# Kernel tuning notes

Measured on AMD Instinct MI355X. Metric: run time of the kernel, lower is better.

The kernel has to match this reference:

```python
import jax, jax.numpy as jnp
import numpy as np

ROPE_BASE = 1000000.0
EPS = 1e-6
N_HEADS = 8


def apply_rope(x, base=ROPE_BASE):
    # x: [b, s, h, d]
    b, s, h, d = x.shape
    half = d // 2
    theta = 1.0 / base ** (2 * jnp.arange(half) / d)          # [half]
    angles = jnp.arange(s)[:, None] * theta[None, :]          # [s, half]
    cos = jnp.cos(angles)[None, :, None, :]                   # [1, s, 1, half]
    sin = jnp.sin(angles)[None, :, None, :]
    x1, x2 = jnp.split(x, 2, axis=-1)
    return jnp.concatenate([x1 * cos - x2 * sin, x1 * sin + x2 * cos], axis=-1)


def setup_inputs() -> dict:
    key = jax.random.key(0)
    ks = jax.random.split(key, 5)
    b, s, dim = 2, 4096, 512
    x = jax.random.normal(ks[0], (b, s, dim), dtype=jnp.float32)
    scale = jnp.ones((dim,), dtype=jnp.float32)
    init = 1.0 / np.sqrt(dim)
    Wq = jax.random.normal(ks[1], (dim, dim), dtype=jnp.float32) * init
    Wk = jax.random.normal(ks[2], (dim, dim), dtype=jnp.float32) * init
    Wv = jax.random.normal(ks[3], (dim, dim), dtype=jnp.float32) * init
    Wo = jax.random.normal(ks[4], (dim, dim), dtype=jnp.float32) * init
    return {"x": x, "scale": scale, "Wq": Wq, "Wk": Wk, "Wv": Wv, "Wo": Wo}


def reference(x, scale, Wq, Wk, Wv, Wo):
    b, s, dim = x.shape
    h = N_HEADS
    dh = dim // h
    # RMSNorm (use_fast_variance=False path)
    variance = jnp.mean(x ** 2, axis=-1, keepdims=True)
    x_norm = x / jnp.sqrt(variance + EPS) * scale
    # Projections (flax Linear: y = x @ kernel, kernel [in, out])
    q = (x_norm @ Wq).reshape(b, s, h, dh)
    k = (x_norm @ Wk).reshape(b, s, h, dh)
    v = (x_norm @ Wv).reshape(b, s, h, dh)
    q = apply_rope(q)
    k = apply_rope(k)
    scores = jnp.einsum('bthd,bshd->bhts', q, k) / jnp.sqrt(jnp.float32(dh))
    mask = jnp.triu(jnp.full((s, s), -jnp.inf, dtype=jnp.float32), k=1)
    scores = scores + mask[None, None, :, :]
    attn = jax.nn.softmax(scores, axis=-1)
    out = jnp.einsum('bhts,bshd->bthd', attn, v).reshape(b, s, dim)
    return out @ Wo
```

## Files before the change

kernel.cpp:

```cpp
#include <hip/hip_runtime.h>
#include <hip/hip_bf16.h>

typedef _Float16 f16;
typedef _Float16 f16x2 __attribute__((ext_vector_type(2)));
typedef _Float16 f16x4 __attribute__((ext_vector_type(4)));
typedef _Float16 f16x8 __attribute__((ext_vector_type(8)));
typedef float f32x4 __attribute__((ext_vector_type(4)));

#define S_LEN 4096
#define DIM   512
#define NH    8
#define DH    64
#define BATCH 2
#define BHDIM (BATCH*NH)

#define QSCALE 0.18033688011112042f

__device__ __forceinline__ void gld16(const f16* g, f16* l) {
#if __has_builtin(__builtin_amdgcn_global_load_lds)
  __builtin_amdgcn_global_load_lds((const __attribute__((address_space(1))) void*)g,
                                   (__attribute__((address_space(3))) void*)l, 16, 0, 0);
#else
  *(f16x8*)l = *(const f16x8*)g;
#endif
}

__device__ __forceinline__ float fexp2(float x) {
#if __has_builtin(__builtin_amdgcn_exp2f)
  return __builtin_amdgcn_exp2f(x);
#else
  return exp2f(x);
#endif
}

__device__ __forceinline__ f16x2 pk2(float a, float b) {
#if __has_builtin(__builtin_amdgcn_cvt_pkrtz)
  auto r = __builtin_amdgcn_cvt_pkrtz(a, b);
  f16x2 o; __builtin_memcpy(&o, &r, sizeof(o));
  return o;
#else
  f16x2 r; r[0] = (f16)a; r[1] = (f16)b; return r;
#endif
}

__global__ __launch_bounds__(256) void prep_kernel(
    const float* __restrict__ x, const float* __restrict__ scale,
    const float* __restrict__ Wq, const float* __restrict__ Wk,
    const float* __restrict__ Wv, const float* __restrict__ Wo,
    f16* __restrict__ xn, f16* __restrict__ wt_qkv, f16* __restrict__ wo_t,
    float* __restrict__ ctab, float* __restrict__ stab) {
  int bid = blockIdx.x;
  int tid = threadIdx.x;
  if (bid < 8192) {
    const float* xr = x + (size_t)bid * DIM;
    float2 v = *(const float2*)(xr + tid*2);
    float ss = v.x*v.x + v.y*v.y;
    #pragma unroll
    for (int off = 32; off > 0; off >>= 1) ss += __shfl_down(ss, off);
    __shared__ float red[4];
    if ((tid & 63) == 0) red[tid >> 6] = ss;
    __syncthreads();
    float tot = red[0] + red[1] + red[2] + red[3];
    float inv = rsqrtf(tot * (1.0f/DIM) + 1e-6f);
    float2 s = *(const float2*)(scale + tid*2);
    xn[(size_t)bid*DIM + tid*2+0] = (f16)(v.x*inv*s.x);
    xn[(size_t)bid*DIM + tid*2+1] = (f16)(v.y*inv*s.y);
  } else if (bid < 9216) {
    __shared__ f16 tile[32][33];
    int b2 = bid - 8192;
    int mat = b2 >> 8;
    int rem = b2 & 255;
    int k0 = (rem >> 4) * 32, n0 = (rem & 15) * 32;
    const float* src = (mat == 0) ? Wq : (mat == 1) ? Wk : (mat == 2) ? Wv : Wo;
    f16* dst = (mat < 3) ? (wt_qkv + (size_t)mat*DIM*DIM) : wo_t;
    int tx = tid & 31, ty = tid >> 5;
    #pragma unroll
    for (int i = 0; i < 32; i += 8)
      tile[ty+i][tx] = (f16)src[(size_t)(k0+ty+i)*DIM + n0+tx];
    __syncthreads();
    #pragma unroll
    for (int i = 0; i < 32; i += 8)
      dst[(size_t)(n0+ty+i)*DIM + k0+tx] = tile[tx][ty+i];
  } else {
    int idx = (bid - 9216)*256 + tid;
    int t = idx >> 5, d = idx & 31;
    float theta = exp2f(-(float)d * (19.931568569324174f / 32.0f));
    float sv, cv;
    sincosf((float)t * theta, &sv, &cv);
    ctab[idx] = cv; stab[idx] = sv;
  }
}

__device__ __forceinline__ void gemm128_acc(
    const f16* __restrict__ A, const f16* __restrict__ Bt,
    int m0, int n0, f16* As, f16* Bs, f32x4 (&acc)[4][4]) {
  const int tid = threadIdx.x;
  const int wave = tid >> 6, lane = tid & 63;
  const int l16 = lane & 15, quad = lane >> 4;
  const int mrow = (wave & 1) * 64, ncol = (wave >> 1) * 64;
  const int srow = tid >> 3;
  const int gc = (tid & 7) ^ ((tid >> 3) & 7);

  for (int k0 = 0; k0 < DIM; k0 += 64) {
    if (k0) __syncthreads();
    #pragma unroll
    for (int i = 0; i < 4; i++) {
      gld16(A  + (size_t)(m0 + i*32 + srow)*DIM + k0 + gc*8, As + i*2048 + tid*8);
      gld16(Bt + (size_t)(n0 + i*32 + srow)*DIM + k0 + gc*8, Bs + i*2048 + tid*8);
    }
    __syncthreads();
    #pragma unroll
    for (int kc = 0; kc < 2; kc++) {
      f16x8 a[4], b[4];
      #pragma unroll
      for (int mt = 0; mt < 4; mt++) {
        int row = mrow + mt*16 + l16;
        a[mt] = *(const f16x8*)(As + row*64 + (((quad + 4*kc) ^ (l16 & 7)) * 8));
      }
      #pragma unroll
      for (int nt = 0; nt < 4; nt++) {
        int row = ncol + nt*16 + l16;
        b[nt] = *(const f16x8*)(Bs + row*64 + (((quad + 4*kc) ^ (l16 & 7)) * 8));
      }
      #pragma unroll
      for (int mt = 0; mt < 4; mt++)
        #pragma unroll
        for (int nt = 0; nt < 4; nt++)
          acc[mt][nt] = __builtin_amdgcn_mfma_f32_16x16x32_f16(a[mt], b[nt], acc[mt][nt], 0, 0, 0);
    }
  }
}

__global__ __launch_bounds__(256) void qkv_gemm_kernel(
    const f16* __restrict__ xn, const f16* __restrict__ wt,
    const float* __restrict__ ctab, const float* __restrict__ stab,
    f16* __restrict__ qbuf, f16* __restrict__ kbuf, f16* __restrict__ vt) {
  __shared__ __align__(16) f16 As[128*64], Bs[128*64];
  int m0 = blockIdx.x * 128, n0 = blockIdx.y * 128;
  f32x4 acc[4][4] = {};
  gemm128_acc(xn, wt, m0, n0, As, Bs, acc);

  const int tid = threadIdx.x;
  const int wave = tid >> 6, lane = tid & 63;
  const int l16 = lane & 15, quad = lane >> 4;
  int ncol = n0 + (wave >> 1) * 64;
  int which = ncol >> 9;
  int head = (ncol >> 6) & 7;
  int mbase = m0 + (wave & 1) * 64;

  if (which <= 1) {
    #pragma unroll
    for (int mt = 0; mt < 4; mt++)
      #pragma unroll
      for (int nt = 0; nt < 2; nt++) {
        int d = nt*16 + l16;
        #pragma unroll
        for (int r = 0; r < 4; r++) {
          int t = (mbase + mt*16 + quad*4 + r) & 4095;
          float cv = ctab[t*32 + d], sv = stab[t*32 + d];
          float x1 = acc[mt][nt][r], x2 = acc[mt][nt+2][r];
          acc[mt][nt][r]   = x1*cv - x2*sv;
          acc[mt][nt+2][r] = x1*sv + x2*cv;
        }
      }
  }
  if (which < 2) {
    float osc = (which == 0) ? QSCALE : 1.0f;
    f16* dst = which ? kbuf : qbuf;
    #pragma unroll
    for (int mt = 0; mt < 4; mt++)
      #pragma unroll
      for (int nt = 0; nt < 4; nt++)
        #pragma unroll
        for (int r = 0; r < 4; r++) {
          int m = mbase + mt*16 + quad*4 + r;
          int b = m >> 12, t = m & 4095;
          dst[(((size_t)(b*NH + head))*S_LEN + t)*DH + nt*16 + l16] = (f16)(acc[mt][nt][r]*osc);
        }
  } else {
    #pragma unroll
    for (int mt = 0; mt < 4; mt++)
      #pragma unroll
      for (int nt = 0; nt < 4; nt++) {
        int m = mbase + mt*16 + quad*4;
        int b = m >> 12, tcol = m & 4095;
        int grp = tcol & ~63;
        int pos = ((mt >> 1)*4 + quad)*8 + (mt & 1)*4;
        int d = nt*16 + l16;
        f16x4 v4 = {(f16)acc[mt][nt][0], (f16)acc[mt][nt][1],
                    (f16)acc[mt][nt][2], (f16)acc[mt][nt][3]};
        *(f16x4*)(vt + ((size_t)((b*NH + head)*DH + d))*S_LEN + grp + pos) = v4;
      }
  }
}

__global__ __launch_bounds__(256, 4) void attn_kernel(
    const f16* __restrict__ qbuf, const f16* __restrict__ kbuf,
    const f16* __restrict__ vtb, f16* __restrict__ ao) {
  int bid = blockIdx.x;
  int bh  = bid & 15;
  int p   = bid >> 4;

  int tid = threadIdx.x;
  int wave = tid >> 6, lane = tid & 63;
  int l16 = lane & 15, quad = lane >> 4;
  int bi = wave >> 1, half = wave & 1;

  const f16* Q = qbuf + (size_t)bh*S_LEN*DH;
  const f16* K = kbuf + (size_t)bh*S_LEN*DH;
  const f16* V = vtb  + (size_t)bh*DH*S_LEN;

  int bv = bi ? p : (127 - p);
  int tc = (bv >> 1) + 1;
  int nth = ((127 - p) >> 1) + 1;
  int rbase = bv*32 + half*16;

  f16x8 qa0, qa1;
  {
    const f16* qrow = Q + (size_t)(rbase + l16)*DH + quad*8;
    qa0 = *(const f16x8*)(qrow);
    qa1 = *(const f16x8*)(qrow + 32);
  }

  f32x4 o[4] = {};
  float m_i = -1e30f;
  float l_i = 0.f;

  __shared__ __align__(16) f16 kt[2*4096];
  __shared__ __align__(16) f16 vs[2*4096];

  const int srow = tid >> 3;
  const int gcs = (tid & 7) ^ (srow & 7);

  #define STAGE(buf, kv)                                                        \
    do {                                                                        \
      f16* ktb = kt + (buf)*4096;                                               \
      f16* vsb = vs + (buf)*4096;                                               \
      _Pragma("unroll")                                                         \
      for (int n = 0; n < 2; n++) {                                             \
        gld16(K + (size_t)((kv) + n*32 + srow)*DH + gcs*8, ktb + n*2048 + tid*8);\
        gld16(V + (size_t)(n*32 + srow)*S_LEN + (kv) + gcs*8, vsb + n*2048 + tid*8);\
      }                                                                         \
    } while (0)

  STAGE(0, 0);
  __syncthreads();

  for (int it = 0; it < nth; ++it) {
    int kv0 = it * 64;
    int cur = it & 1;
    if (it + 1 < nth) STAGE(cur ^ 1, kv0 + 64);

    const f16* ktc = kt + cur*4096;
    const f16* vsc = vs + cur*4096;

    if (it < tc) {
      bool diag = (it == tc - 1);
      int ntl = diag ? ((bv & 1) ? 4 : 2) : 4;
      int kcl = ntl >> 1;

      f32x4 st[4];
      #pragma unroll
      for (int nt = 0; nt < 4; nt++) {
        if (nt >= ntl) continue;
        int row = nt*16 + l16;
        f16x8 kf0 = *(const f16x8*)(ktc + row*64 + (((quad)     ^ (row & 7))*8));
        f16x8 kf1 = *(const f16x8*)(ktc + row*64 + (((quad + 4) ^ (row & 7))*8));
        f32x4 z = {};
        z = __builtin_amdgcn_mfma_f32_16x16x32_f16(kf0, qa0, z, 0, 0, 0);
        st[nt] = __builtin_amdgcn_mfma_f32_16x16x32_f16(kf1, qa1, z, 0, 0, 0);
      }

      int qglob = rbase + l16;
      float rmx = -1e30f;
      #pragma unroll
      for (int nt = 0; nt < 4; nt++) {
        if (nt >= ntl) continue;
        if (diag) {
          int kb = kv0 + nt*16 + quad*4;
          #pragma unroll
          for (int r = 0; r < 4; r++) {
            float v = st[nt][r];
            if (kb + r > qglob) v = -1e30f;
            st[nt][r] = v;
            rmx = fmaxf(rmx, v);
          }
        } else {
          #pragma unroll
          for (int r = 0; r < 4; r++) rmx = fmaxf(rmx, st[nt][r]);
        }
      }
      rmx = fmaxf(rmx, __shfl_xor(rmx, 16));
      rmx = fmaxf(rmx, __shfl_xor(rmx, 32));
      if (!__all(rmx <= m_i + 8.0f)) {
        float mnew = fmaxf(m_i, rmx);
        float alpha = fexp2(m_i - mnew);
        m_i = mnew;
        float al[4];
        #pragma unroll
        for (int r = 0; r < 4; r++) al[r] = __shfl(alpha, quad*4 + r);
        #pragma unroll
        for (int dnt = 0; dnt < 4; dnt++)
          #pragma unroll
          for (int r = 0; r < 4; r++) o[dnt][r] *= al[r];
        l_i *= alpha;
      }
      float mref = m_i;
      float rs = 0.f;
      f16x8 pa[2];
      #pragma unroll
      for (int c = 0; c < 2; c++) {
        if (c >= kcl) continue;
        float e0 = fexp2(st[2*c  ][0] - mref);
        float e1 = fexp2(st[2*c  ][1] - mref);
        float e2 = fexp2(st[2*c  ][2] - mref);
        float e3 = fexp2(st[2*c  ][3] - mref);
        float e4 = fexp2(st[2*c+1][0] - mref);
        float e5 = fexp2(st[2*c+1][1] - mref);
        float e6 = fexp2(st[2*c+1][2] - mref);
        float e7 = fexp2(st[2*c+1][3] - mref);
        rs += ((e0+e1)+(e2+e3)) + ((e4+e5)+(e6+e7));
        f16x4 h0 = __builtin_shufflevector(pk2(e0,e1), pk2(e2,e3), 0,1,2,3);
        f16x4 h1 = __builtin_shufflevector(pk2(e4,e5), pk2(e6,e7), 0,1,2,3);
        pa[c] = __builtin_shufflevector(h0, h1, 0,1,2,3,4,5,6,7);
      }
      l_i += rs;

      #pragma unroll
      for (int c = 0; c < 2; c++) {
        if (c >= kcl) continue;
        #pragma unroll
        for (int dnt = 0; dnt < 4; dnt++) {
          int vr = dnt*16 + l16;
          f16x8 vf = *(const f16x8*)(vsc + vr*64 + (((c*4 + quad) ^ (vr & 7))*8));
          o[dnt] = __builtin_amdgcn_mfma_f32_16x16x32_f16(pa[c], vf, o[dnt], 0, 0, 0);
        }
      }
    }

    __syncthreads();
  }
  #undef STAGE

  int b = bh >> 3, h = bh & 7;
  {
    float lf = l_i;
    lf += __shfl_xor(lf, 16);
    lf += __shfl_xor(lf, 32);
    float lr[4];
    #pragma unroll
    for (int r = 0; r < 4; r++) lr[r] = __shfl(lf, quad*4 + r);
    #pragma unroll
    for (int r = 0; r < 4; r++) {
      float invl = 1.0f / lr[r];
      int t = rbase + quad*4 + r;
      size_t rowoff = ((size_t)(b*S_LEN + t))*DIM + h*DH;
      #pragma unroll
      for (int dnt = 0; dnt < 4; dnt++)
        ao[rowoff + dnt*16 + l16] = (f16)(o[dnt][r]*invl);
    }
  }
}

__global__ __launch_bounds__(256) void out_gemm_kernel(
    const f16* __restrict__ ao, const f16* __restrict__ wot,
    float* __restrict__ out) {
  __shared__ __align__(16) f16 As[128*64], Bs[128*64];
  int m0 = blockIdx.x * 128, n0 = blockIdx.y * 128;
  f32x4 acc[4][4] = {};
  gemm128_acc(ao, wot, m0, n0, As, Bs, acc);

  const int tid = threadIdx.x;
  const int wave = tid >> 6, lane = tid & 63;
  const int l16 = lane & 15, quad = lane >> 4;
  int ncol = n0 + (wave >> 1) * 64;
  int mbase = m0 + (wave & 1) * 64;
  #pragma unroll
  for (int mt = 0; mt < 4; mt++)
    #pragma unroll
    for (int nt = 0; nt < 4; nt++)
      #pragma unroll
      for (int r = 0; r < 4; r++)
        out[(size_t)(mbase + mt*16 + quad*4 + r)*DIM + ncol + nt*16 + l16] = acc[mt][nt][r];
}

extern "C" void kernel_launch(void* const* d_in, const int* in_sizes, int n_in,
                              void* d_out, int out_size, void* d_ws, size_t ws_size,
                              hipStream_t stream) {
  const float* x     = (const float*)d_in[0];
  const float* scale = (const float*)d_in[1];
  const float* Wq    = (const float*)d_in[2];
  const float* Wk    = (const float*)d_in[3];
  const float* Wv    = (const float*)d_in[4];
  const float* Wo    = (const float*)d_in[5];
  float* out = (float*)d_out;

  const size_t ROWS = (size_t)BATCH * S_LEN;
  char* ws = (char*)d_ws;
  f16* xn     = (f16*)ws;  ws += ROWS * DIM * sizeof(f16);
  f16* wt_qkv = (f16*)ws;  ws += (size_t)3 * DIM * DIM * sizeof(f16);
  f16* wo_t   = (f16*)ws;  ws += (size_t)DIM * DIM * sizeof(f16);
  f16* qb     = (f16*)ws;  ws += (size_t)BHDIM * S_LEN * DH * sizeof(f16);
  f16* kb     = (f16*)ws;  ws += (size_t)BHDIM * S_LEN * DH * sizeof(f16);
  f16* vt     = (f16*)ws;  ws += (size_t)BHDIM * S_LEN * DH * sizeof(f16);
  float* ctab = (float*)ws; ws += (size_t)S_LEN * 32 * sizeof(float);
  float* stab = (float*)ws; ws += (size_t)S_LEN * 32 * sizeof(float);
  f16* ao     = xn;

  size_t need = (size_t)(ws - (char*)d_ws);
  if (ws_size < need) return;

  prep_kernel    <<<9728, 256, 0, stream>>>(x, scale, Wq, Wk, Wv, Wo,
                                            xn, wt_qkv, wo_t, ctab, stab);
  qkv_gemm_kernel<<<dim3(64,12), 256, 0, stream>>>(xn, wt_qkv, ctab, stab, qb, kb, vt);
  attn_kernel    <<<1024, 256, 0, stream>>>(qb, kb, vt, ao);
  out_gemm_kernel<<<dim3(64,4), 256, 0, stream>>>(ao, wo_t, out);
}
```

Baseline: 192.6 us.

## Split attention KV loop across two blocks and merge partial softmax results

Each attention block now handles every other KV tile (even or odd), so twice as many blocks run, each over about half the keys. Each block writes normalized partial outputs plus the row max and sum to workspace. A new merge kernel rescales and combines the two halves into the head-interleaved layout. The aim is more parallelism and occupancy (launch bounds raised to 5) and a shorter critical path, at the cost of extra global traffic for the partials and one more kernel launch.

```diff
diff --git a/kernel.cpp b/kernel.cpp
--- a/kernel.cpp
+++ b/kernel.cpp
@@ -13,6 +13,7 @@
 #define DH    64
 #define BATCH 2
 #define BHDIM (BATCH*NH)
+#define ROWS2 (BHDIM*S_LEN)
 
 #define QSCALE 0.18033688011112042f
 
@@ -194,12 +195,14 @@
   }
 }
 
-__global__ __launch_bounds__(256, 4) void attn_kernel(
+__global__ __launch_bounds__(256, 5) void attn_kernel(
     const f16* __restrict__ qbuf, const f16* __restrict__ kbuf,
-    const f16* __restrict__ vtb, f16* __restrict__ ao) {
+    const f16* __restrict__ vtb, f16* __restrict__ po,
+    float* __restrict__ pm, float* __restrict__ pl) {
   int bid = blockIdx.x;
   int bh  = bid & 15;
-  int p   = bid >> 4;
+  int hf  = (bid >> 4) & 1;
+  int p   = bid >> 5;
 
   int tid = threadIdx.x;
   int wave = tid >> 6, lane = tid & 63;
@@ -212,7 +215,8 @@
 
   int bv = bi ? p : (127 - p);
   int tc = (bv >> 1) + 1;
-  int nth = ((127 - p) >> 1) + 1;
+  int T0 = ((127 - p) >> 1) + 1;
+  int nloc = (T0 - hf + 1) >> 1;
   int rbase = bv*32 + half*16;
 
   f16x8 qa0, qa1;
@@ -243,19 +247,20 @@
       }                                                                         \
     } while (0)
 
-  STAGE(0, 0);
+  STAGE(0, hf*64);
   __syncthreads();
 
-  for (int it = 0; it < nth; ++it) {
-    int kv0 = it * 64;
-    int cur = it & 1;
-    if (it + 1 < nth) STAGE(cur ^ 1, kv0 + 64);
+  for (int itl = 0; itl < nloc; ++itl) {
+    int g = 2*itl + hf;
+    int kv0 = g * 64;
+    int cur = itl & 1;
+    if (itl + 1 < nloc) STAGE(cur ^ 1, kv0 + 128);
 
     const f16* ktc = kt + cur*4096;
     const f16* vsc = vs + cur*4096;
 
-    if (it < tc) {
-      bool diag = (it == tc - 1);
+    if (g < tc) {
+      bool diag = (g == tc - 1);
       int ntl = diag ? ((bv & 1) ? 4 : 2) : 4;
       int kcl = ntl >> 1;
 
@@ -342,24 +347,57 @@
   }
   #undef STAGE
 
-  int b = bh >> 3, h = bh & 7;
   {
     float lf = l_i;
     lf += __shfl_xor(lf, 16);
     lf += __shfl_xor(lf, 32);
+    if (quad == 0) {
+      int t = rbase + l16;
+      pm[(size_t)(hf*BHDIM + bh)*S_LEN + t] = m_i;
+      pl[(size_t)(hf*BHDIM + bh)*S_LEN + t] = lf;
+    }
     float lr[4];
     #pragma unroll
     for (int r = 0; r < 4; r++) lr[r] = __shfl(lf, quad*4 + r);
     #pragma unroll
     for (int r = 0; r < 4; r++) {
-      float invl = 1.0f / lr[r];
+      float invl = (lr[r] > 0.f) ? 1.0f / lr[r] : 0.f;
       int t = rbase + quad*4 + r;
-      size_t rowoff = ((size_t)(b*S_LEN + t))*DIM + h*DH;
+      size_t rowoff = ((size_t)(hf*BHDIM + bh)*S_LEN + t)*DH;
       #pragma unroll
       for (int dnt = 0; dnt < 4; dnt++)
-        ao[rowoff + dnt*16 + l16] = (f16)(o[dnt][r]*invl);
+        po[rowoff + dnt*16 + l16] = (f16)(o[dnt][r]*invl);
     }
   }
+}
+
+__global__ __launch_bounds__(256) void merge_kernel(
+    const f16* __restrict__ po, const float* __restrict__ pm,
+    const float* __restrict__ pl, f16* __restrict__ ao) {
+  int idx = blockIdx.x*256 + threadIdx.x;
+  int r_ = idx >> 2, q = idx & 3;
+  int bh = r_ >> 12, t = r_ & 4095;
+  float m0 = pm[r_], m1 = pm[ROWS2 + r_];
+  float l0 = pl[r_], l1 = pl[ROWS2 + r_];
+  float M  = fmaxf(m0, m1);
+  float a0 = l0 * fexp2(m0 - M);
+  float a1 = l1 * fexp2(m1 - M);
+  float inv = 1.0f / (a0 + a1);
+  float w0 = a0 * inv, w1 = a1 * inv;
+  const f16* p0 = po + (size_t)r_*DH + q*16;
+  const f16* p1 = po + (size_t)(ROWS2 + r_)*DH + q*16;
+  int b = bh >> 3, h = bh & 7;
+  f16* dst = ao + ((size_t)(b*S_LEN + t))*DIM + h*DH + q*16;
+  f16x8 v0a = *(const f16x8*)(p0), v0b = *(const f16x8*)(p0 + 8);
+  f16x8 v1a = *(const f16x8*)(p1), v1b = *(const f16x8*)(p1 + 8);
+  f16x8 oa, ob;
+  #pragma unroll
+  for (int j = 0; j < 8; j++) {
+    oa[j] = (f16)(w0*(float)v0a[j] + w1*(float)v1a[j]);
+    ob[j] = (f16)(w0*(float)v0b[j] + w1*(float)v1b[j]);
+  }
+  *(f16x8*)dst = oa;
+  *(f16x8*)(dst + 8) = ob;
 }
 
 __global__ __launch_bounds__(256) void out_gemm_kernel(
@@ -405,6 +443,9 @@
   f16* vt     = (f16*)ws;  ws += (size_t)BHDIM * S_LEN * DH * sizeof(f16);
   float* ctab = (float*)ws; ws += (size_t)S_LEN * 32 * sizeof(float);
   float* stab = (float*)ws; ws += (size_t)S_LEN * 32 * sizeof(float);
+  f16* po     = (f16*)ws;  ws += (size_t)2 * ROWS2 * DH * sizeof(f16);
+  float* pm   = (float*)ws; ws += (size_t)2 * ROWS2 * sizeof(float);
+  float* pl   = (float*)ws; ws += (size_t)2 * ROWS2 * sizeof(float);
   f16* ao     = xn;
 
   size_t need = (size_t)(ws - (char*)d_ws);
@@ -413,6 +454,7 @@
   prep_kernel    <<<9728, 256, 0, stream>>>(x, scale, Wq, Wk, Wv, Wo,
                                             xn, wt_qkv, wo_t, ctab, stab);
   qkv_gemm_kernel<<<dim3(64,12), 256, 0, stream>>>(xn, wt_qkv, ctab, stab, qb, kb, vt);
-  attn_kernel    <<<1024, 256, 0, stream>>>(qb, kb, vt, ao);
+  attn_kernel    <<<2048, 256, 0, stream>>>(qb, kb, vt, po, pm, pl);
+  merge_kernel   <<<1024, 256, 0, stream>>>(po, pm, pl, ao);
   out_gemm_kernel<<<dim3(64,4), 256, 0, stream>>>(ao, wo_t, out);
 }
```

Measured after the change: 189.4 us. No clear change (-1.7%).
